# Performance work log

Hardware: AMD Instinct MI355X
Metric: run time of the kernel (lower is better)

Reference implementation:

```python
import jax, jax.numpy as jnp
import numpy as np

B, N, D, H, DH = 4, 1024, 1024, 16, 64
INNER = H * DH  # 1024


def setup_inputs() -> dict:
    key = jax.random.key(0)
    k0, k1, k2, k3 = jax.random.split(key, 4)
    x = jax.random.normal(k0, (B, N, D), dtype=jnp.float32)
    # float 0/1 padding mask per token
    mask = jax.random.randint(k1, (B, N), 0, 2).astype(jnp.float32)
    w_qkv = jax.random.normal(k2, (D, 3 * INNER), dtype=jnp.float32) * (D ** -0.5)
    w_out = jax.random.normal(k3, (INNER, D), dtype=jnp.float32) * (INNER ** -0.5)
    b_out = jnp.zeros((D,), dtype=jnp.float32)
    return {"x": x, "mask": mask, "w_qkv": w_qkv, "w_out": w_out, "b_out": b_out}


def reference(x, mask, w_qkv, w_out, b_out):
    scale = DH ** -0.5
    qkv = x @ w_qkv  # [B,N,3*INNER]
    q, k, v = jnp.split(qkv, 3, axis=-1)
    resh = lambda t: t.reshape(B, N, H, DH).transpose(0, 2, 1, 3)  # b h n d
    q, k, v = resh(q), resh(k), resh(v)
    dots = jnp.einsum('bhnd,bhmd->bhnm', q, k) * scale  # [B,H,N,N]
    # attn_bias = 1 - m_i*m_j; blocked where isclose(attn_bias, 1) i.e. pair ~ 0
    pair = mask[:, None, :, None] * mask[:, None, None, :]  # [B,1,N,N]
    blocked = jnp.isclose(1.0 - pair, jnp.ones_like(pair))
    dots = jnp.where(blocked, -jnp.inf, dots)
    # fully-masked-row fixup: rows that are all -inf get dots=0, attn forced to 0
    valid = jnp.any(dots != -jnp.inf, axis=-1, keepdims=True)  # [B,H,N,1]
    dots = jnp.where(valid, dots, 0.0)
    attn = jax.nn.softmax(dots, axis=-1)
    attn = jnp.where(valid, attn, 0.0)
    out = jnp.einsum('bhnm,bhmd->bhnd', attn, v)
    out = out.transpose(0, 2, 1, 3).reshape(B, N, INNER)
    return out @ w_out + b_out
```

## Files before the change

### kernel.cpp

```cpp
#include <hip/hip_runtime.h>

#define INF __builtin_inff()

typedef __attribute__((ext_vector_type(8))) short bf16x8;
typedef __attribute__((ext_vector_type(4))) short s16x4;
typedef __attribute__((ext_vector_type(4))) float f32x4;
typedef __attribute__((ext_vector_type(8))) unsigned short u16x8;
typedef __attribute__((ext_vector_type(4))) unsigned short u16x4;

#define MFMA16(a, b, c) __builtin_amdgcn_mfma_f32_16x16x32_bf16(a, b, c, 0, 0, 0)

#define ASYNC16(g, l) __builtin_amdgcn_global_load_lds( \
    (const __attribute__((address_space(1))) unsigned int*)(const void*)(g), \
    (__attribute__((address_space(3))) unsigned int*)(void*)(l), 16, 0, 0)

#if __has_builtin(__builtin_amdgcn_exp2f)
#define EXP2(x) __builtin_amdgcn_exp2f(x)
#else
#define EXP2(x) exp2f(x)
#endif

#define QSCALE 0.18033688011112042f

__device__ __forceinline__ unsigned short f2bf(float f) {
  union { float f; unsigned u; } v; v.f = f;
  unsigned r = v.u + 0x7fffu + ((v.u >> 16) & 1u);
  return (unsigned short)(r >> 16);
}

__global__ __launch_bounds__(256) void k_prep(
    const float* __restrict__ x, const float* __restrict__ mask,
    const float* __restrict__ wqkv, const float* __restrict__ wout,
    unsigned short* __restrict__ xc, unsigned short* __restrict__ wqkvt,
    unsigned short* __restrict__ woutt, unsigned short* __restrict__ perm,
    int* __restrict__ nvb, const float* __restrict__ bias, float* __restrict__ C) {
  __shared__ union {
    float tile[32][33];
    struct { unsigned short lperm[1024]; int wtot[4]; } sc;
  } sh;
  const int lid = blockIdx.x;
  const int t = threadIdx.x, lane = t & 63, wid = t >> 6;

  if (lid >= 5124) {
    const int idx = lid - 5124;
    const int b = idx >> 6, g = idx & 63;
    const float4 bv = ((const float4*)bias)[t];
    const float* mrow = mask + b * 1024 + g * 16;
#pragma unroll
    for (int j = 0; j < 16; ++j) {
      if (mrow[j] == 0.f)
        ((float4*)(C + ((size_t)(b * 1024 + g * 16 + j)) * 1024))[t] = bv;
    }
    return;
  }

  if (lid >= 4 && lid < 4100) {
    int id = lid - 4;
    const float* src; unsigned short* dst; int Cc, bc, br;
    if (id < 3072) { src = wqkv; dst = wqkvt; Cc = 3072; bc = (id % 96) * 32; br = (id / 96) * 32; }
    else { id -= 3072; src = wout; dst = woutt; Cc = 1024; bc = (id & 31) * 32; br = (id >> 5) * 32; }
    const int tx = t & 31, ty = t >> 5;
#pragma unroll
    for (int i = 0; i < 32; i += 8)
      sh.tile[ty + i][tx] = src[(size_t)(br + ty + i) * Cc + bc + tx];
    __syncthreads();
#pragma unroll
    for (int i = 0; i < 32; i += 8)
      dst[(size_t)(bc + ty + i) * 1024 + br + tx] = f2bf(sh.tile[tx][ty + i]);
    return;
  }

  const int b = (lid < 4) ? lid : ((lid - 4100) >> 8);
  float4 mv = ((const float4*)(mask + b * 1024))[t];
  int v0 = mv.x != 0.f, v1 = mv.y != 0.f, v2 = mv.z != 0.f, v3 = mv.w != 0.f;
  int cnt = v0 + v1 + v2 + v3;
  int pre = cnt;
#pragma unroll
  for (int d = 1; d < 64; d <<= 1) { int n = __shfl_up(pre, d); if (lane >= d) pre += n; }
  if (lane == 63) sh.sc.wtot[wid] = pre;
  __syncthreads();
  int base = 0;
#pragma unroll
  for (int i = 0; i < 4; ++i) if (i < wid) base += sh.sc.wtot[i];
  const int nvt = sh.sc.wtot[0] + sh.sc.wtot[1] + sh.sc.wtot[2] + sh.sc.wtot[3];
  int ex = base + pre - cnt;
  int vv[4] = { v0, v1, v2, v3 };

  if (lid < 4) {
#pragma unroll
    for (int j = 0; j < 4; ++j) {
      int tok = t * 4 + j;
      if (vv[j]) { perm[b * 1024 + ex] = (unsigned short)tok; ++ex; }
      else         perm[b * 1024 + nvt + (tok - ex)] = (unsigned short)tok;
    }
    if (t == 0) nvb[b] = nvt;
    return;
  }

#pragma unroll
  for (int j = 0; j < 4; ++j) {
    int tok = t * 4 + j;
    if (vv[j]) { sh.sc.lperm[ex] = (unsigned short)tok; ++ex; }
  }
  __syncthreads();
  const int s0 = ((lid - 4100) & 255) * 4;
  const int ce = (nvt + 127) & ~127;
#pragma unroll
  for (int j = 0; j < 4; ++j) {
    int slot = s0 + j;
    if (slot >= ce) continue;
    u16x4 o;
    if (slot < nvt) {
      int tok = sh.sc.lperm[slot];
      float4 f = ((const float4*)(x + ((size_t)(b * 1024 + tok)) * 1024))[t];
      o[0] = f2bf(f.x); o[1] = f2bf(f.y); o[2] = f2bf(f.z); o[3] = f2bf(f.w);
    } else {
      o[0] = o[1] = o[2] = o[3] = 0;
    }
    ((u16x4*)(xc + ((size_t)(b * 1024 + slot)) * 1024))[t] = o;
  }
}

__global__ __launch_bounds__(256) void k_gemm_qkv(
    const unsigned short* __restrict__ A, const unsigned short* __restrict__ Bt,
    const int* __restrict__ nvb,
    unsigned short* __restrict__ qcmp, unsigned short* __restrict__ kcmp,
    unsigned short* __restrict__ vt) {
  __shared__ unsigned short SH[32768];
  const int lid = blockIdx.x;
  const int xcd = lid & 7, i6 = lid >> 3;
  const int colt = xcd * 3 + (i6 % 3);
  const int rowt = i6 / 3;
  const int b = rowt >> 3, mt = rowt & 7;
  const int nv = nvb[b];
  if (mt * 128 >= nv) return;
  const int bm0 = mt * 128;
  const int bn0 = colt * 128;
  const size_t abase = ((size_t)(b * 1024 + bm0)) * 1024;
  const int t = threadIdx.x;
  const int lane = t & 63, wave = t >> 6;
  const int wm = (wave >> 1) * 64, wn = (wave & 1) * 64;
  const int lr = lane & 15, quad = lane >> 4;
  const int sw = lr & 7;
  f32x4 acc[4][4] = {};
  auto stage = [&](int pp, int k0) {
    unsigned short* As = SH + pp * 16384;
    unsigned short* Bs = As + 8192;
#pragma unroll
    for (int j = 0; j < 4; ++j) {
      int idx = t + j * 256;
      int row = idx >> 3;
      int g = (idx ^ row) & 7;
      ASYNC16(&A[abase + (size_t)row * 1024 + k0 + g * 8], &As[idx * 8]);
      ASYNC16(&Bt[((size_t)(bn0 + row)) * 1024 + k0 + g * 8], &Bs[idx * 8]);
    }
  };
  stage(0, 0);
  for (int it = 0; it < 16; ++it) {
    const int pp = it & 1;
    __syncthreads();
    if (it + 1 < 16) stage(1 - pp, (it + 1) * 64);
    const unsigned short* As = SH + pp * 16384;
    const unsigned short* Bs = As + 8192;
#pragma unroll
    for (int ks = 0; ks < 2; ++ks) {
      bf16x8 af[4], bfr[4];
#pragma unroll
      for (int i = 0; i < 4; ++i)
        af[i] = *(const bf16x8*)(&As[(wm + i * 16 + lr) * 64 + (((ks * 4 + quad) ^ sw)) * 8]);
#pragma unroll
      for (int j = 0; j < 4; ++j)
        bfr[j] = *(const bf16x8*)(&Bs[(wn + j * 16 + lr) * 64 + (((ks * 4 + quad) ^ sw)) * 8]);
#pragma unroll
      for (int i = 0; i < 4; ++i)
#pragma unroll
        for (int j = 0; j < 4; ++j)
          acc[i][j] = MFMA16(af[i], bfr[j], acc[i][j]);
    }
  }
  const int sec = bn0 >> 10;
  const int js0 = bn0 & 1023;
  const float qs = (sec == 0) ? QSCALE : 1.f;
#pragma unroll
  for (int hh = 0; hh < 2; ++hh) {
    __syncthreads();
    if ((wave >> 1) == hh) {
#pragma unroll
      for (int i = 0; i < 4; ++i)
#pragma unroll
        for (int j = 0; j < 4; ++j)
#pragma unroll
          for (int r = 0; r < 4; ++r)
            SH[(i * 16 + quad * 4 + r) * 136 + wn + j * 16 + lr] = f2bf(acc[i][j][r] * qs);
    }
    __syncthreads();
    if (sec < 2) {
      unsigned short* dstT = sec ? kcmp : qcmp;
#pragma unroll
      for (int rr = 0; rr < 4; ++rr) {
        int lrow = (t >> 4) + rr * 16;
        int ck = t & 15;
        int slot = bm0 + hh * 64 + lrow;
        int js = js0 + ck * 8;
        int h = js >> 6, d = js & 63;
        u16x8 v = *(u16x8*)(&SH[lrow * 136 + ck * 8]);
        *(u16x8*)(&dstT[(((size_t)(b * 16 + h)) * 1024 + slot) * 64 + d]) = v;
      }
    } else {
      const int c = t & 127, seg = t >> 7;
      const int js = js0 + c, h = js >> 6, d = js & 63;
      unsigned short* vrow =
          &vt[(((size_t)(b * 16 + h)) * 64 + d) * 1024 + bm0 + hh * 64 + seg * 32];
#pragma unroll
      for (int s4 = 0; s4 < 4; ++s4) {
        u16x8 v;
#pragma unroll
        for (int s = 0; s < 8; ++s) v[s] = SH[(seg * 32 + s4 * 8 + s) * 136 + c];
        *(u16x8*)(vrow + s4 * 8) = v;
      }
    }
  }
}

__global__ __launch_bounds__(256, 3) void k_attn(
    const unsigned short* __restrict__ qcmp, const unsigned short* __restrict__ kcmp,
    const unsigned short* __restrict__ vtc, const int* __restrict__ nvb,
    unsigned short* __restrict__ aoc) {
  __shared__ unsigned short Ks[2][4096];
  __shared__ unsigned short Vs[2][4096];
  __shared__ unsigned short P[4][16 * 72];
  const int bx = blockIdx.x;
  const int bh = (bx & 7) + 8 * (bx >> 7);
  const int qcb = (bx >> 3) & 15;
  const int b = bh >> 4;
  const int nv = nvb[b];
  if (qcb * 64 >= nv) return;
  const int t = threadIdx.x;
  const int wave = t >> 6, lane = t & 63;
  const int lr = lane & 15, quad = lane >> 4;
  const int q0 = qcb * 64 + wave * 16;
  const unsigned short* qp = qcmp + ((size_t)bh << 16);
  const unsigned short* kp = kcmp + ((size_t)bh << 16);
  const unsigned short* vp = vtc + ((size_t)bh << 16);
  unsigned short* Pw = P[wave];
  bf16x8 qv0 = *(const bf16x8*)(qp + (q0 + lr) * 64 + quad * 8);
  bf16x8 qv1 = *(const bf16x8*)(qp + (q0 + lr) * 64 + 32 + quad * 8);
  float m = -INF, l = 0.f;
  f32x4 o[4] = {};
  const int sw = lr & 7;
  const int nk = (nv + 63) >> 6;
  auto stage = [&](int pp, int kc0) {
#pragma unroll
    for (int ld = 0; ld < 2; ++ld) {
      int idx = t + ld * 256;
      int row = idx >> 3;
      int g = (idx ^ row) & 7;
      ASYNC16(kp + (kc0 + row) * 64 + g * 8, &Ks[pp][idx * 8]);
      ASYNC16(vp + (size_t)row * 1024 + kc0 + g * 8, &Vs[pp][idx * 8]);
    }
  };
  stage(0, 0);
  for (int it = 0; it < nk; ++it) {
    const int pp = it & 1;
    const int kc0 = it * 64;
    __syncthreads();
    if (it + 1 < nk) stage(1 - pp, kc0 + 64);
    f32x4 st[4];
    __builtin_amdgcn_s_setprio(1);
#pragma unroll
    for (int tt = 0; tt < 4; ++tt) {
      int krow = tt * 16 + lr;
      bf16x8 k0 = *(const bf16x8*)(&Ks[pp][krow * 64 + ((quad ^ sw)) * 8]);
      bf16x8 k1 = *(const bf16x8*)(&Ks[pp][krow * 64 + (((4 + quad) ^ sw)) * 8]);
      f32x4 c = {};
      c = MFMA16(k0, qv0, c);
      c = MFMA16(k1, qv1, c);
      st[tt] = c;
    }
    __builtin_amdgcn_s_setprio(0);
    float tm = -INF;
    if (kc0 + 64 <= nv) {
#pragma unroll
      for (int tt = 0; tt < 4; ++tt)
#pragma unroll
        for (int r = 0; r < 4; ++r) tm = fmaxf(tm, st[tt][r]);
    } else {
#pragma unroll
      for (int tt = 0; tt < 4; ++tt)
#pragma unroll
        for (int r = 0; r < 4; ++r) {
          int slot = kc0 + tt * 16 + quad * 4 + r;
          float v = (slot < nv) ? st[tt][r] : -INF;
          st[tt][r] = v;
          tm = fmaxf(tm, v);
        }
    }
    tm = fmaxf(tm, __shfl_xor(tm, 16));
    tm = fmaxf(tm, __shfl_xor(tm, 32));
    float mn = fmaxf(m, tm);
    const bool resc = !__all(tm <= m + 8.f);
    if (!resc) mn = m;
    float ps = 0.f;
#pragma unroll
    for (int tt = 0; tt < 4; ++tt) {
      s16x4 pv;
#pragma unroll
      for (int r = 0; r < 4; ++r) {
        float pe = EXP2(st[tt][r] - mn);
        ps += pe;
        pv[r] = (short)f2bf(pe);
      }
      *(s16x4*)(&Pw[lr * 72 + tt * 16 + quad * 4]) = pv;
    }
    ps += __shfl_xor(ps, 16);
    ps += __shfl_xor(ps, 32);
    if (resc) {
      float alpha = EXP2(m - mn);
      l = l * alpha + ps;
      m = mn;
      float ar[4];
#pragma unroll
      for (int r = 0; r < 4; ++r) ar[r] = __shfl(alpha, quad * 4 + r);
#pragma unroll
      for (int jj = 0; jj < 4; ++jj)
#pragma unroll
        for (int r = 0; r < 4; ++r) o[jj][r] *= ar[r];
    } else {
      l += ps;
    }
    __builtin_amdgcn_s_setprio(1);
#pragma unroll
    for (int sh = 0; sh < 2; ++sh) {
      bf16x8 pa = *(const bf16x8*)(&Pw[lr * 72 + sh * 32 + quad * 8]);
#pragma unroll
      for (int jj = 0; jj < 4; ++jj) {
        bf16x8 vbf = *(const bf16x8*)(&Vs[pp][(jj * 16 + lr) * 64 + (((sh * 4 + quad) ^ sw)) * 8]);
        o[jj] = MFMA16(pa, vbf, o[jj]);
      }
    }
    __builtin_amdgcn_s_setprio(0);
  }
  float inv = 1.f / l;
  float ir[4];
#pragma unroll
  for (int r = 0; r < 4; ++r) ir[r] = __shfl(inv, quad * 4 + r);
#pragma unroll
  for (int jj = 0; jj < 4; ++jj)
#pragma unroll
    for (int r = 0; r < 4; ++r)
      Pw[(quad * 4 + r) * 72 + jj * 16 + lr] = f2bf(o[jj][r] * ir[r]);
  const int h = bh & 15;
  const int slot = q0 + lr;
  if (slot < nv) {
    size_t rowb = ((size_t)(b * 1024 + slot)) * 1024 + h * 64;
#pragma unroll
    for (int p = 0; p < 2; ++p) {
      u16x8 v8 = *(const u16x8*)(&Pw[lr * 72 + (quad + p * 4) * 8]);
      *(u16x8*)(&aoc[rowb + (quad + p * 4) * 8]) = v8;
    }
  }
}

__global__ __launch_bounds__(256) void k_gemm_fin(
    const unsigned short* __restrict__ A, const unsigned short* __restrict__ Bt,
    const unsigned short* __restrict__ perm, const int* __restrict__ nvb,
    const float* __restrict__ bias, float* __restrict__ C) {
  __shared__ unsigned short SH[24576];
  const int lid = blockIdx.x;
  const int t = threadIdx.x;
  const int col = lid & 7;
  const int rt = lid >> 3;
  const int b = rt >> 4, mt = rt & 15;
  const int nv = nvb[b];
  if (mt * 64 >= nv) return;
  const int bm0 = mt * 64;
  const int bn0 = col * 128;
  const size_t abase = ((size_t)(b * 1024 + bm0)) * 1024;
  const int lane = t & 63, wave = t >> 6;
  const int wm = (wave >> 1) * 32, wn = (wave & 1) * 64;
  const int lr = lane & 15, quad = lane >> 4;
  const int sw = lr & 7;
  f32x4 acc[2][4] = {};
  auto stage = [&](int pp, int k0) {
    unsigned short* As = SH + pp * 12288;
    unsigned short* Bs = As + 4096;
#pragma unroll
    for (int j = 0; j < 2; ++j) {
      int idx = t + j * 256;
      int row = idx >> 3;
      int g = (idx ^ row) & 7;
      ASYNC16(&A[abase + (size_t)row * 1024 + k0 + g * 8], &As[idx * 8]);
    }
#pragma unroll
    for (int j = 0; j < 4; ++j) {
      int idx = t + j * 256;
      int row = idx >> 3;
      int g = (idx ^ row) & 7;
      ASYNC16(&Bt[((size_t)(bn0 + row)) * 1024 + k0 + g * 8], &Bs[idx * 8]);
    }
  };
  stage(0, 0);
  for (int it = 0; it < 16; ++it) {
    const int pp = it & 1;
    __syncthreads();
    if (it + 1 < 16) stage(1 - pp, (it + 1) * 64);
    const unsigned short* As = SH + pp * 12288;
    const unsigned short* Bs = As + 4096;
#pragma unroll
    for (int ks = 0; ks < 2; ++ks) {
      bf16x8 af[2], bfr[4];
#pragma unroll
      for (int i = 0; i < 2; ++i)
        af[i] = *(const bf16x8*)(&As[(wm + i * 16 + lr) * 64 + (((ks * 4 + quad) ^ sw)) * 8]);
#pragma unroll
      for (int j = 0; j < 4; ++j)
        bfr[j] = *(const bf16x8*)(&Bs[(wn + j * 16 + lr) * 64 + (((ks * 4 + quad) ^ sw)) * 8]);
#pragma unroll
      for (int i = 0; i < 2; ++i)
#pragma unroll
        for (int j = 0; j < 4; ++j)
          acc[i][j] = MFMA16(af[i], bfr[j], acc[i][j]);
    }
  }
  __syncthreads();
  float* W = (float*)SH + wave * 2176;
  float bj[4];
#pragma unroll
  for (int j = 0; j < 4; ++j) bj[j] = bias[bn0 + wn + j * 16 + lr];
#pragma unroll
  for (int i = 0; i < 2; ++i)
#pragma unroll
    for (int j = 0; j < 4; ++j)
#pragma unroll
      for (int r = 0; r < 4; ++r)
        W[(i * 16 + quad * 4 + r) * 68 + j * 16 + lr] = acc[i][j][r] + bj[j];
#pragma unroll
  for (int p = 0; p < 8; ++p) {
    int fi = p * 64 + lane;
    int row = fi >> 4, c4 = fi & 15;
    int slot = bm0 + wm + row;
    if (slot < nv) {
      int tok = perm[b * 1024 + slot];
      float4 v4 = *(const float4*)(&W[row * 68 + c4 * 4]);
      *(float4*)(&C[((size_t)(b * 1024 + tok)) * 1024 + bn0 + wn + c4 * 4]) = v4;
    }
  }
}

extern "C" void kernel_launch(void* const* d_in, const int* in_sizes, int n_in,
                              void* d_out, int out_size, void* d_ws, size_t ws_size,
                              hipStream_t stream) {
  const float* x    = (const float*)d_in[0];
  const float* mask = (const float*)d_in[1];
  const float* wqkv = (const float*)d_in[2];
  const float* wout = (const float*)d_in[3];
  const float* bout = (const float*)d_in[4];
  float* out = (float*)d_out;
  char* ws = (char*)d_ws;
  unsigned short* xc    = (unsigned short*)(ws);
  unsigned short* aoc   = (unsigned short*)(ws);
  unsigned short* wqkvt = (unsigned short*)(ws + (size_t)( 8 << 20));
  unsigned short* woutt = (unsigned short*)(ws + (size_t)(14 << 20));
  unsigned short* qcmp  = (unsigned short*)(ws + (size_t)(16 << 20));
  unsigned short* kcmp  = (unsigned short*)(ws + (size_t)(24 << 20));
  unsigned short* vt    = (unsigned short*)(ws + (size_t)(32 << 20));
  unsigned short* perm  = (unsigned short*)(ws + (size_t)(40 << 20));
  int*            nvb   = (int*)           (ws + (size_t)(40 << 20) + 8192);

  k_prep<<<5380, 256, 0, stream>>>(x, mask, wqkv, wout, xc, wqkvt, woutt, perm, nvb, bout, out);
  k_gemm_qkv<<<768, 256, 0, stream>>>(xc, wqkvt, nvb, qcmp, kcmp, vt);
  k_attn<<<1024, 256, 0, stream>>>(qcmp, kcmp, vt, nvb, aoc);
  k_gemm_fin<<<512, 256, 0, stream>>>(aoc, woutt, perm, nvb, bout, out);
}
```

Baseline: 142.9 us.

## Enlarge attention query tile to 128 rows and shrink output-GEMM N tile

The attention kernel now runs 512 threads (8 waves) per block over 128 query rows, so each staged K/V tile in shared memory is reused by twice as many query rows and K/V global traffic is halved. The output projection GEMM halves its N tile to 64 columns, doubles the grid, maps blocks so each XCD handles adjacent column pairs, and requests 4 blocks per CU. The aim is more parallelism and occupancy in the final GEMM, at the cost of re-reading the A tile more often. The epilogue now goes through one shared staging tile with an extra barrier.

```diff
diff --git a/kernel.cpp b/kernel.cpp
--- a/kernel.cpp
+++ b/kernel.cpp
@@ -222,23 +222,23 @@
   }
 }
 
-__global__ __launch_bounds__(256, 3) void k_attn(
+__global__ __launch_bounds__(512) void k_attn(
     const unsigned short* __restrict__ qcmp, const unsigned short* __restrict__ kcmp,
     const unsigned short* __restrict__ vtc, const int* __restrict__ nvb,
     unsigned short* __restrict__ aoc) {
   __shared__ unsigned short Ks[2][4096];
   __shared__ unsigned short Vs[2][4096];
-  __shared__ unsigned short P[4][16 * 72];
+  __shared__ unsigned short P[8][16 * 72];
   const int bx = blockIdx.x;
-  const int bh = (bx & 7) + 8 * (bx >> 7);
-  const int qcb = (bx >> 3) & 15;
+  const int bh = (bx & 7) + 8 * (bx >> 6);
+  const int qcb = (bx >> 3) & 7;
   const int b = bh >> 4;
   const int nv = nvb[b];
-  if (qcb * 64 >= nv) return;
+  if (qcb * 128 >= nv) return;
   const int t = threadIdx.x;
   const int wave = t >> 6, lane = t & 63;
   const int lr = lane & 15, quad = lane >> 4;
-  const int q0 = qcb * 64 + wave * 16;
+  const int q0 = qcb * 128 + wave * 16;
   const unsigned short* qp = qcmp + ((size_t)bh << 16);
   const unsigned short* kp = kcmp + ((size_t)bh << 16);
   const unsigned short* vp = vtc + ((size_t)bh << 16);
@@ -250,14 +250,10 @@
   const int sw = lr & 7;
   const int nk = (nv + 63) >> 6;
   auto stage = [&](int pp, int kc0) {
-#pragma unroll
-    for (int ld = 0; ld < 2; ++ld) {
-      int idx = t + ld * 256;
-      int row = idx >> 3;
-      int g = (idx ^ row) & 7;
-      ASYNC16(kp + (kc0 + row) * 64 + g * 8, &Ks[pp][idx * 8]);
-      ASYNC16(vp + (size_t)row * 1024 + kc0 + g * 8, &Vs[pp][idx * 8]);
-    }
+    int row = t >> 3;
+    int g = (t ^ row) & 7;
+    ASYNC16(kp + (kc0 + row) * 64 + g * 8, &Ks[pp][t * 8]);
+    ASYNC16(vp + (size_t)row * 1024 + kc0 + g * 8, &Vs[pp][t * 8]);
   };
   stage(0, 0);
   for (int it = 0; it < nk; ++it) {
@@ -361,28 +357,29 @@
   }
 }
 
-__global__ __launch_bounds__(256) void k_gemm_fin(
+__global__ __launch_bounds__(256, 4) void k_gemm_fin(
     const unsigned short* __restrict__ A, const unsigned short* __restrict__ Bt,
     const unsigned short* __restrict__ perm, const int* __restrict__ nvb,
     const float* __restrict__ bias, float* __restrict__ C) {
-  __shared__ unsigned short SH[24576];
+  __shared__ unsigned short SH[16384];
   const int lid = blockIdx.x;
   const int t = threadIdx.x;
-  const int col = lid & 7;
-  const int rt = lid >> 3;
-  const int b = rt >> 4, mt = rt & 15;
+  const int xcd = lid & 7, i7 = lid >> 3;
+  const int col = xcd * 2 + (i7 & 1);
+  const int rowt = i7 >> 1;
+  const int b = rowt >> 4, mt = rowt & 15;
   const int nv = nvb[b];
   if (mt * 64 >= nv) return;
   const int bm0 = mt * 64;
-  const int bn0 = col * 128;
+  const int bn0 = col * 64;
   const size_t abase = ((size_t)(b * 1024 + bm0)) * 1024;
   const int lane = t & 63, wave = t >> 6;
-  const int wm = (wave >> 1) * 32, wn = (wave & 1) * 64;
+  const int wm = (wave >> 1) * 32, wn = (wave & 1) * 32;
   const int lr = lane & 15, quad = lane >> 4;
   const int sw = lr & 7;
-  f32x4 acc[2][4] = {};
+  f32x4 acc[2][2] = {};
   auto stage = [&](int pp, int k0) {
-    unsigned short* As = SH + pp * 12288;
+    unsigned short* As = SH + pp * 8192;
     unsigned short* Bs = As + 4096;
 #pragma unroll
     for (int j = 0; j < 2; ++j) {
@@ -390,12 +387,6 @@
       int row = idx >> 3;
       int g = (idx ^ row) & 7;
       ASYNC16(&A[abase + (size_t)row * 1024 + k0 + g * 8], &As[idx * 8]);
-    }
-#pragma unroll
-    for (int j = 0; j < 4; ++j) {
-      int idx = t + j * 256;
-      int row = idx >> 3;
-      int g = (idx ^ row) & 7;
       ASYNC16(&Bt[((size_t)(bn0 + row)) * 1024 + k0 + g * 8], &Bs[idx * 8]);
     }
   };
@@ -404,45 +395,46 @@
     const int pp = it & 1;
     __syncthreads();
     if (it + 1 < 16) stage(1 - pp, (it + 1) * 64);
-    const unsigned short* As = SH + pp * 12288;
+    const unsigned short* As = SH + pp * 8192;
     const unsigned short* Bs = As + 4096;
 #pragma unroll
     for (int ks = 0; ks < 2; ++ks) {
-      bf16x8 af[2], bfr[4];
+      bf16x8 af[2], bfr[2];
 #pragma unroll
       for (int i = 0; i < 2; ++i)
         af[i] = *(const bf16x8*)(&As[(wm + i * 16 + lr) * 64 + (((ks * 4 + quad) ^ sw)) * 8]);
 #pragma unroll
-      for (int j = 0; j < 4; ++j)
+      for (int j = 0; j < 2; ++j)
         bfr[j] = *(const bf16x8*)(&Bs[(wn + j * 16 + lr) * 64 + (((ks * 4 + quad) ^ sw)) * 8]);
 #pragma unroll
       for (int i = 0; i < 2; ++i)
 #pragma unroll
-        for (int j = 0; j < 4; ++j)
+        for (int j = 0; j < 2; ++j)
           acc[i][j] = MFMA16(af[i], bfr[j], acc[i][j]);
     }
   }
   __syncthreads();
-  float* W = (float*)SH + wave * 2176;
-  float bj[4];
-#pragma unroll
-  for (int j = 0; j < 4; ++j) bj[j] = bias[bn0 + wn + j * 16 + lr];
+  float* W = (float*)SH;
+  float bj[2];
+#pragma unroll
+  for (int j = 0; j < 2; ++j) bj[j] = bias[bn0 + wn + j * 16 + lr];
 #pragma unroll
   for (int i = 0; i < 2; ++i)
 #pragma unroll
-    for (int j = 0; j < 4; ++j)
+    for (int j = 0; j < 2; ++j)
 #pragma unroll
       for (int r = 0; r < 4; ++r)
-        W[(i * 16 + quad * 4 + r) * 68 + j * 16 + lr] = acc[i][j][r] + bj[j];
-#pragma unroll
-  for (int p = 0; p < 8; ++p) {
-    int fi = p * 64 + lane;
+        W[(wm + i * 16 + quad * 4 + r) * 68 + wn + j * 16 + lr] = acc[i][j][r] + bj[j];
+  __syncthreads();
+#pragma unroll
+  for (int p = 0; p < 4; ++p) {
+    int fi = p * 256 + t;
     int row = fi >> 4, c4 = fi & 15;
-    int slot = bm0 + wm + row;
+    int slot = bm0 + row;
     if (slot < nv) {
       int tok = perm[b * 1024 + slot];
       float4 v4 = *(const float4*)(&W[row * 68 + c4 * 4]);
-      *(float4*)(&C[((size_t)(b * 1024 + tok)) * 1024 + bn0 + wn + c4 * 4]) = v4;
+      *(float4*)(&C[((size_t)(b * 1024 + tok)) * 1024 + bn0 + c4 * 4]) = v4;
     }
   }
 }
@@ -469,6 +461,6 @@
 
   k_prep<<<5380, 256, 0, stream>>>(x, mask, wqkv, wout, xc, wqkvt, woutt, perm, nvb, bout, out);
   k_gemm_qkv<<<768, 256, 0, stream>>>(xc, wqkvt, nvb, qcmp, kcmp, vt);
-  k_attn<<<1024, 256, 0, stream>>>(qcmp, kcmp, vt, nvb, aoc);
-  k_gemm_fin<<<512, 256, 0, stream>>>(aoc, woutt, perm, nvb, bout, out);
-}
+  k_attn<<<512, 512, 0, stream>>>(qcmp, kcmp, vt, nvb, aoc);
+  k_gemm_fin<<<1024, 256, 0, stream>>>(aoc, woutt, perm, nvb, bout, out);
+}
```

New measurement: 145.9 us. 2.1% more time.
